# Performance work log

Hardware: AMD Instinct MI355X
Metric: run time of the kernel (lower is better)

The kernel has to match this reference:

```python
import jax, jax.numpy as jnp
import numpy as np

B, L, DIM = 2, 2048, 1024
H, DH, W = 16, 64, 256  # heads, head_dim, window_size
ROPE_BASE = 10000.0


def _rope(x):
    # x: [b, l, h, d] -> rotate consecutive pairs (torch view_as_complex semantics)
    l, d = x.shape[1], x.shape[3]
    freqs = 1.0 / (ROPE_BASE ** (jnp.arange(0, d, 2, dtype=jnp.float32) / d))  # [d/2]
    ang = jnp.arange(l, dtype=jnp.float32)[:, None] * freqs[None, :]           # [l, d/2]
    cos = jnp.cos(ang)[None, :, None, :].astype(x.dtype)
    sin = jnp.sin(ang)[None, :, None, :].astype(x.dtype)
    xe, xo = x[..., 0::2], x[..., 1::2]
    ye = xe * cos - xo * sin
    yo = xe * sin + xo * cos
    return jnp.stack([ye, yo], axis=-1).reshape(x.shape)


def setup_inputs() -> dict:
    key = jax.random.key(0)
    ks = jax.random.split(key, 7)
    sh = (B, L, DIM)
    return {
        "q": jax.random.normal(ks[0], sh, jnp.float32),
        "k": jax.random.normal(ks[1], sh, jnp.float32),
        "v": jax.random.normal(ks[2], sh, jnp.float32),
        "wq": jax.random.normal(ks[3], (H * DH, DIM), jnp.float32) * 0.02,
        "wk": jax.random.normal(ks[4], (H * DH, DIM), jnp.float32) * 0.02,
        "wv": jax.random.normal(ks[5], (H * DH, DIM), jnp.float32) * 0.02,
        "wo": jax.random.normal(ks[6], (DIM, H * DH), jnp.float32) * 0.02,
    }


def reference(q, k, v, wq, wk, wv, wo):
    b, l, _ = q.shape
    qh = (q @ wq.T).reshape(b, l, H, DH)
    kh = (k @ wk.T).reshape(b, l, H, DH)
    vh = (v @ wv.T).reshape(b, l, H, DH).transpose(0, 2, 1, 3)  # [b,h,l,d]
    qh = _rope(qh).transpose(0, 2, 1, 3)                        # [b,h,l,d]
    kh = _rope(kh).transpose(0, 2, 1, 3)
    scores = jnp.einsum('bhqd,bhkd->bhqk', qh, kh) * (DH ** -0.5)
    i = jnp.arange(l)[:, None]
    j = jnp.arange(l)[None, :]
    window_mask = (j <= i) & (j >= i - W)  # keys in [i-W, i], matches the loop
    scores = jnp.where(window_mask, scores, -1e30)
    probs = jax.nn.softmax(scores, axis=-1)
    out = jnp.einsum('bhqk,bhkd->bhqd', probs, vh)
    out = out.transpose(0, 2, 1, 3).reshape(b, l, H * DH)
    return out @ wo.T
```

## Files before the change

kernel.cpp:

```cpp
#include <hip/hip_runtime.h>
#include <stdint.h>

#define B_    2
#define L_    2048
#define DIM_  1024
#define H_    16
#define DH_   64
#define WWIN  256

typedef __attribute__((ext_vector_type(4))) float f32x4;
typedef __attribute__((ext_vector_type(8))) short bf16x8;

__device__ __forceinline__ unsigned short f2bf(float x) {
  union { float f; unsigned u; } c; c.f = x;
  unsigned r = c.u + 0x7fffu + ((c.u >> 16) & 1u);
  return (unsigned short)(r >> 16);
}

struct CastArgs {
  const float* src[7];
  unsigned short* dst[7];
};
__global__ __launch_bounds__(256) void cast_bf16_kernel(CastArgs a) {
  int bid = blockIdx.x;
  int arr, base;
  if (bid < 12288) {
    arr = bid >> 12;
    base = (bid & 4095) << 10;
  } else {
    int t = bid - 12288;
    arr = 3 + (t >> 10);
    base = (t & 1023) << 10;
  }
  int i = base + (int)threadIdx.x * 4;
  float4 v = *(const float4*)(a.src[arr] + i);
  ushort4 o;
  o.x = f2bf(v.x); o.y = f2bf(v.y); o.z = f2bf(v.z); o.w = f2bf(v.w);
  *(ushort4*)(a.dst[arr] + i) = o;
}

#define BM 128
#define BN 64
#define BK 64

__device__ __forceinline__ void gld_lds16(const void* g, void* l) {
  __builtin_amdgcn_global_load_lds(
      (const __attribute__((address_space(1))) void*)g,
      (__attribute__((address_space(3))) void*)l, 16, 0, 0);
}

__device__ __forceinline__ void gemm_core_1024(
    const unsigned short* __restrict__ A, const unsigned short* __restrict__ Bt,
    unsigned short* As, unsigned short* Bs, f32x4 (&acc)[2][4],
    int m0, int n0) {
  const int tid = threadIdx.x;
  const int wave = tid >> 6, lane = tid & 63;
  const int quad = lane >> 4, l16 = lane & 15;
  const int srow = tid >> 3, sc = tid & 7;

  auto stage = [&](int k0, int buf) {
    unsigned short* Ad = As + buf * 8192;
    unsigned short* Bd = Bs + buf * 4096;
    #pragma unroll
    for (int rd = 0; rd < 4; ++rd) {
      int row = rd * 32 + srow;
      int cs = sc ^ (row & 7);
      gld_lds16(A + (size_t)(m0 + row) * 1024 + k0 + cs * 8, Ad + row * BK + sc * 8);
    }
    #pragma unroll
    for (int rd = 0; rd < 2; ++rd) {
      int row = rd * 32 + srow;
      int cs = sc ^ (row & 7);
      gld_lds16(Bt + (size_t)(n0 + row) * 1024 + k0 + cs * 8, Bd + row * BK + sc * 8);
    }
  };

  stage(0, 0);
  for (int k = 0; k < 16; ++k) {
    const int cur = k & 1;
    __syncthreads();
    if (k < 15) stage((k + 1) * BK, cur ^ 1);
    const unsigned short* Ac = As + cur * 8192;
    const unsigned short* Bc = Bs + cur * 4096;
    #pragma unroll
    for (int ks = 0; ks < 2; ++ks) {
      bf16x8 af[2], bfr[4];
      #pragma unroll
      for (int i = 0; i < 2; ++i) {
        int row = wave * 32 + i * 16 + l16;
        int ch = (ks * 4 + quad) ^ (row & 7);
        af[i] = *(const bf16x8*)(Ac + row * BK + ch * 8);
      }
      #pragma unroll
      for (int j = 0; j < 4; ++j) {
        int row = j * 16 + l16;
        int ch = (ks * 4 + quad) ^ (row & 7);
        bfr[j] = *(const bf16x8*)(Bc + row * BK + ch * 8);
      }
      #pragma unroll
      for (int i = 0; i < 2; ++i)
        #pragma unroll
        for (int j = 0; j < 4; ++j)
          acc[i][j] = __builtin_amdgcn_mfma_f32_16x16x32_bf16(af[i], bfr[j], acc[i][j], 0, 0, 0);
    }
  }
}

struct ProjArgs {
  const unsigned short* A[3];
  const unsigned short* Bt[3];
  unsigned short* C[3];
};
__global__ __launch_bounds__(256) void gemm_proj_kernel(ProjArgs pa) {
  __shared__ unsigned short SH[24576];
  unsigned short* As = SH;
  unsigned short* Bs = SH + 16384;

  const int bflat = blockIdx.x;
  const int xcd = bflat & 7, s = bflat >> 3;
  const int nblk = s & 15;
  const int mz = xcd * 12 + (s >> 4);
  const int z = mz >> 5;
  const int mblk = mz & 31;
  const int m0 = mblk * BM, n0 = nblk * BN;

  f32x4 acc[2][4] = {};
  gemm_core_1024(pa.A[z], pa.Bt[z], As, Bs, acc, m0, n0);

  const int tid = threadIdx.x;
  const int lane = tid & 63, wave = tid >> 6;
  const int quad = lane >> 4, l16 = lane & 15;

  if (z < 2) {
    float frev[4];
    #pragma unroll
    for (int j = 0; j < 4; ++j) {
      int d = j * 16 + l16;
      frev[j] = exp2f(-(float)(d >> 1) * 0.41524101186092029f) * 0.15915494309189535f;
    }
    unsigned short* C = pa.C[z];
    const int h = nblk;
    const bool even = (l16 & 1) == 0;
    #pragma unroll
    for (int i = 0; i < 2; ++i)
      #pragma unroll
      for (int r = 0; r < 4; ++r) {
        int m = m0 + wave * 32 + i * 16 + quad * 4 + r;
        int b = m >> 11, l = m & (L_ - 1);
        float lf = (float)l;
        #pragma unroll
        for (int j = 0; j < 4; ++j) {
          int d = j * 16 + l16;
          float v = acc[i][j][r];
          float p = __shfl_xor(v, 1);
          float a = lf * frev[j];
          float t = a - floorf(a);
          float sn = __builtin_amdgcn_sinf(t);
          float cs = __builtin_amdgcn_cosf(t);
          float o = even ? (v * cs - p * sn) : (p * sn + v * cs);
          C[(((size_t)b * H_ + h) * L_ + l) * DH_ + d] = f2bf(o);
        }
      }
  } else {
    __syncthreads();
    unsigned short* T = SH + wave * 2304;
    #pragma unroll
    for (int i = 0; i < 2; ++i)
      #pragma unroll
      for (int j = 0; j < 4; ++j) {
        int nw = j * 16 + l16;
        int hm = i * 4 + quad;
        uint2 pk;
        pk.x = (unsigned)f2bf(acc[i][j][0]) | ((unsigned)f2bf(acc[i][j][1]) << 16);
        pk.y = (unsigned)f2bf(acc[i][j][2]) | ((unsigned)f2bf(acc[i][j][3]) << 16);
        *(uint2*)(T + nw * 36 + hm * 4) = pk;
      }
    asm volatile("s_waitcnt lgkmcnt(0)" ::: "memory");
    int h = nblk;
    int d = lane;
    int b = m0 >> 11;
    int lbase = (m0 & (L_ - 1)) + wave * 32;
    unsigned short* C = pa.C[2];
    size_t rowbase = (((size_t)b * H_ + h) * DH_ + d) * L_ + lbase;
    #pragma unroll
    for (int t = 0; t < 4; ++t) {
      uint2 lo = *(uint2*)(T + lane * 36 + t * 8);
      uint2 hi = *(uint2*)(T + lane * 36 + t * 8 + 4);
      uint4 o = {lo.x, lo.y, hi.x, hi.y};
      *(uint4*)(C + rowbase + t * 8) = o;
    }
  }
}

__global__ __launch_bounds__(256) void gemm_out_kernel(
    const unsigned short* __restrict__ A, const unsigned short* __restrict__ Bt,
    float* __restrict__ C) {
  __shared__ unsigned short SH[24576];
  unsigned short* As = SH;
  unsigned short* Bs = SH + 16384;

  const int bflat = blockIdx.x;
  const int xcd = bflat & 7, s = bflat >> 3;
  const int nblk = s & 15;
  const int mblk = xcd * 4 + (s >> 4);
  const int m0 = mblk * BM, n0 = nblk * BN;

  f32x4 acc[2][4] = {};
  gemm_core_1024(A, Bt, As, Bs, acc, m0, n0);

  const int lane = threadIdx.x & 63, wave = threadIdx.x >> 6;
  const int quad = lane >> 4, l16 = lane & 15;
  #pragma unroll
  for (int i = 0; i < 2; ++i)
    #pragma unroll
    for (int j = 0; j < 4; ++j)
      #pragma unroll
      for (int r = 0; r < 4; ++r) {
        int m = m0 + wave * 32 + i * 16 + quad * 4 + r;
        int n = n0 + j * 16 + l16;
        C[(size_t)m * DIM_ + n] = acc[i][j][r];
      }
}

#define VSTR 336
__global__ __launch_bounds__(256) void attn_kernel(
    const unsigned short* __restrict__ Qh,
    const unsigned short* __restrict__ Kh,
    const unsigned short* __restrict__ Vt,
    unsigned short* __restrict__ O) {
  __shared__ unsigned short Vs[64 * VSTR];
  const int tid = threadIdx.x;
  const int wave = tid >> 6, lane = tid & 63;
  const int quad = lane >> 4, l16 = lane & 15;

  const int bflat = blockIdx.x;
  const int xcd = bflat & 7, s = bflat >> 3;
  const int qt = s >> 2;
  const int bh = xcd * 4 + (s & 3);

  const int q0 = qt * 64;
  const int qb = q0 + wave * 16;
  const int kw0 = qb - WWIN;
  const bool edge = (kw0 < 0);

  const unsigned short* vbase = Vt + (size_t)bh * DH_ * L_;
  #pragma unroll
  for (int it = 0; it < 11; ++it) {
    if (it * 256 + wave * 64 < 2688) {
      int ci = it * 256 + tid;
      int row = ci / 42, ch = ci - row * 42;
      int key0 = q0 - WWIN + ch * 8;
      key0 = key0 < 0 ? 0 : key0;
      key0 = key0 > (L_ - 8) ? (L_ - 8) : key0;
      gld_lds16(vbase + (size_t)row * L_ + key0, Vs + ci * 8);
    }
  }

  bf16x8 qf0, qf1;
  {
    const unsigned short* qrow = Qh + ((size_t)bh * L_ + qb + l16) * DH_;
    qf0 = *(const bf16x8*)(qrow + quad * 8);
    qf1 = *(const bf16x8*)(qrow + 32 + quad * 8);
  }

  f32x4 S[17] = {};
  const unsigned short* kbase = Kh + (size_t)bh * L_ * DH_;
  #pragma unroll
  for (int c = 0; c < 17; ++c) {
    int key = kw0 + c * 16 + l16;
    key = key < 0 ? 0 : key;
    const unsigned short* kr = kbase + (size_t)key * DH_ + quad * 8;
    bf16x8 kf0 = *(const bf16x8*)(kr);
    bf16x8 kf1 = *(const bf16x8*)(kr + 32);
    S[c] = __builtin_amdgcn_mfma_f32_16x16x32_bf16(kf0, qf0, S[c], 0, 0, 0);
    S[c] = __builtin_amdgcn_mfma_f32_16x16x32_bf16(kf1, qf1, S[c], 0, 0, 0);
  }

  const int off16 = quad * 4;
  #pragma unroll
  for (int r = 0; r < 4; ++r) {
    if (off16 + r < l16)  S[0][r]  = -1e30f;
    if (off16 + r > l16)  S[16][r] = -1e30f;
  }
  if (edge) {
    #pragma unroll
    for (int c = 0; c < 17; ++c)
      #pragma unroll
      for (int r = 0; r < 4; ++r)
        if (kw0 + c * 16 + off16 + r < 0) S[c][r] = -1e30f;
  }

  float mx = -1e30f;
  #pragma unroll
  for (int c = 0; c < 17; ++c)
    #pragma unroll
    for (int r = 0; r < 4; ++r)
      mx = fmaxf(mx, S[c][r]);
  mx = fmaxf(mx, __shfl_xor(mx, 16));
  mx = fmaxf(mx, __shfl_xor(mx, 32));
  float sum = 0.f;
  #pragma unroll
  for (int c = 0; c < 17; ++c)
    #pragma unroll
    for (int r = 0; r < 4; ++r) {
      float e = __builtin_amdgcn_exp2f((S[c][r] - mx) * 0.18033688011112042f);
      S[c][r] = e;
      sum += e;
    }
  sum += __shfl_xor(sum, 16);
  sum += __shfl_xor(sum, 32);
  const float ivl = 1.0f / sum;

  __syncthreads();

  f32x4 Oacc[4] = {};
  const int srcA = (lane & 15) | ((lane & 16) << 1);
  const int srcB = srcA + 16;
  const bool loq = quad < 2;
  #pragma unroll
  for (int g = 0; g < 9; ++g) {
    unsigned uA0, uA1, uB0, uB1;
    {
      float a0 = S[2 * g][0] * ivl, a1 = S[2 * g][1] * ivl;
      float a2 = S[2 * g][2] * ivl, a3 = S[2 * g][3] * ivl;
      asm("v_cvt_pk_bf16_f32 %0, %1, %2" : "=v"(uA0) : "v"(a0), "v"(a1));
      asm("v_cvt_pk_bf16_f32 %0, %1, %2" : "=v"(uA1) : "v"(a2), "v"(a3));
    }
    if (g < 8) {
      float b0 = S[2 * g + 1][0] * ivl, b1 = S[2 * g + 1][1] * ivl;
      float b2 = S[2 * g + 1][2] * ivl, b3 = S[2 * g + 1][3] * ivl;
      asm("v_cvt_pk_bf16_f32 %0, %1, %2" : "=v"(uB0) : "v"(b0), "v"(b1));
      asm("v_cvt_pk_bf16_f32 %0, %1, %2" : "=v"(uB1) : "v"(b2), "v"(b3));
    } else {
      uB0 = 0; uB1 = 0;
    }
    unsigned tA0a = __shfl(uA0, srcA), tA1a = __shfl(uA1, srcA);
    unsigned tB0a = __shfl(uB0, srcA), tB1a = __shfl(uB1, srcA);
    unsigned tA0b = __shfl(uA0, srcB), tA1b = __shfl(uA1, srcB);
    unsigned tB0b = __shfl(uB0, srcB), tB1b = __shfl(uB1, srcB);
    union { unsigned u[4]; bf16x8 v; } pa;
    pa.u[0] = loq ? tA0a : tB0a;
    pa.u[1] = loq ? tA1a : tB1a;
    pa.u[2] = loq ? tA0b : tB0b;
    pa.u[3] = loq ? tA1b : tB1b;
    const int kloc = wave * 16 + g * 32 + quad * 8;
    #pragma unroll
    for (int t = 0; t < 4; ++t) {
      bf16x8 vf = *(const bf16x8*)(&Vs[(t * 16 + l16) * VSTR + kloc]);
      Oacc[t] = __builtin_amdgcn_mfma_f32_16x16x32_bf16(pa.v, vf, Oacc[t], 0, 0, 0);
    }
  }

  int b = bh >> 4, h = bh & 15;
  #pragma unroll
  for (int t = 0; t < 4; ++t)
    #pragma unroll
    for (int r = 0; r < 4; ++r) {
      int l = qb + quad * 4 + r;
      int col = h * DH_ + t * 16 + l16;
      O[((size_t)b * L_ + l) * (H_ * DH_) + col] = f2bf(Oacc[t][r]);
    }
}

extern "C" void kernel_launch(void* const* d_in, const int* in_sizes, int n_in,
                              void* d_out, int out_size, void* d_ws, size_t ws_size,
                              hipStream_t stream) {
  const float* q  = (const float*)d_in[0];
  const float* k  = (const float*)d_in[1];
  const float* v  = (const float*)d_in[2];
  const float* wq = (const float*)d_in[3];
  const float* wk = (const float*)d_in[4];
  const float* wv = (const float*)d_in[5];
  const float* wo = (const float*)d_in[6];

  const size_t SA = (size_t)B_ * L_ * DIM_;
  const size_t SW = (size_t)DIM_ * DIM_;
  unsigned short* w   = (unsigned short*)d_ws;
  unsigned short* qb  = w; w += SA;
  unsigned short* kb  = w; w += SA;
  unsigned short* vb  = w; w += SA;
  unsigned short* wqb = w; w += SW;
  unsigned short* wkb = w; w += SW;
  unsigned short* wvb = w; w += SW;
  unsigned short* wob = w; w += SW;
  unsigned short* qh  = w; w += SA;
  unsigned short* kh  = w; w += SA;
  unsigned short* vt  = w; w += SA;
  unsigned short* Ob  = w; w += SA;

  CastArgs ca;
  ca.src[0] = q;  ca.dst[0] = qb;
  ca.src[1] = k;  ca.dst[1] = kb;
  ca.src[2] = v;  ca.dst[2] = vb;
  ca.src[3] = wq; ca.dst[3] = wqb;
  ca.src[4] = wk; ca.dst[4] = wkb;
  ca.src[5] = wv; ca.dst[5] = wvb;
  ca.src[6] = wo; ca.dst[6] = wob;
  cast_bf16_kernel<<<dim3(16384), 256, 0, stream>>>(ca);

  ProjArgs pa;
  pa.A[0] = qb; pa.Bt[0] = wqb; pa.C[0] = qh;
  pa.A[1] = kb; pa.Bt[1] = wkb; pa.C[1] = kh;
  pa.A[2] = vb; pa.Bt[2] = wvb; pa.C[2] = vt;
  gemm_proj_kernel<<<dim3(16 * 32 * 3), 256, 0, stream>>>(pa);

  attn_kernel<<<dim3(32 * 32), 256, 0, stream>>>(qh, kh, vt, Ob);
  gemm_out_kernel<<<dim3(16 * 32), 256, 0, stream>>>(Ob, wob, (float*)d_out);
}
```

Before: 183.6 us.

## Use 128x128 BK32 tiles for QKV projection and swizzle attention V tile

The QKV projection GEMM moves from 128x64 tiles with BK=64 to 128x128 tiles with BK=32 on a 2x2 wave grid. This halves the block count and doubles the reuse of each A tile, and the V-transpose epilogue is rewritten around an XOR-swizzled LDS staging area. The attention kernel's V tile in LDS drops its padded stride (336 to 320) and uses an XOR swizzle on chunk index to avoid bank conflicts, and the final g==8 chunk index is clamped. The cost is more accumulator registers per thread (64 floats), which may lower occupancy, and only 768 blocks to fill the device.

Result: slower. 189.6 us (+3.2%).

```diff
diff --git a/kernel.cpp b/kernel.cpp
--- a/kernel.cpp
+++ b/kernel.cpp
@@ -49,6 +49,62 @@
       (__attribute__((address_space(3))) void*)l, 16, 0, 0);
 }
 
+__device__ __forceinline__ void gemm_core_128x128_bk32(
+    const unsigned short* __restrict__ A, const unsigned short* __restrict__ Bt,
+    unsigned short* As, unsigned short* Bs, f32x4 (&acc)[4][4],
+    int m0, int n0) {
+  const int tid = threadIdx.x;
+  const int wave = tid >> 6, lane = tid & 63;
+  const int quad = lane >> 4, l16 = lane & 15;
+  const int wm = wave >> 1, wn = wave & 1;
+
+  auto stage = [&](int k0, int buf) {
+    unsigned short* Ad = As + buf * 4096;
+    unsigned short* Bd = Bs + buf * 4096;
+    #pragma unroll
+    for (int rd = 0; rd < 2; ++rd) {
+      int ci = rd * 256 + tid;
+      int row = ci >> 2, ch = ci & 3;
+      int gch = ch ^ (row & 3);
+      gld_lds16(A + (size_t)(m0 + row) * 1024 + k0 + gch * 8, Ad + ci * 8);
+    }
+    #pragma unroll
+    for (int rd = 0; rd < 2; ++rd) {
+      int ci = rd * 256 + tid;
+      int row = ci >> 2, ch = ci & 3;
+      int gch = ch ^ (row & 3);
+      gld_lds16(Bt + (size_t)(n0 + row) * 1024 + k0 + gch * 8, Bd + ci * 8);
+    }
+  };
+
+  stage(0, 0);
+  for (int k = 0; k < 32; ++k) {
+    const int cur = k & 1;
+    __syncthreads();
+    if (k < 31) stage((k + 1) * 32, cur ^ 1);
+    const unsigned short* Ac = As + cur * 4096;
+    const unsigned short* Bc = Bs + cur * 4096;
+    bf16x8 af[4], bfr[4];
+    #pragma unroll
+    for (int i = 0; i < 4; ++i) {
+      int row = wm * 64 + i * 16 + l16;
+      int slot = quad ^ (row & 3);
+      af[i] = *(const bf16x8*)(Ac + row * 32 + slot * 8);
+    }
+    #pragma unroll
+    for (int j = 0; j < 4; ++j) {
+      int row = wn * 64 + j * 16 + l16;
+      int slot = quad ^ (row & 3);
+      bfr[j] = *(const bf16x8*)(Bc + row * 32 + slot * 8);
+    }
+    #pragma unroll
+    for (int i = 0; i < 4; ++i)
+      #pragma unroll
+      for (int j = 0; j < 4; ++j)
+        acc[i][j] = __builtin_amdgcn_mfma_f32_16x16x32_bf16(af[i], bfr[j], acc[i][j], 0, 0, 0);
+  }
+}
+
 __device__ __forceinline__ void gemm_core_1024(
     const unsigned short* __restrict__ A, const unsigned short* __restrict__ Bt,
     unsigned short* As, unsigned short* Bs, f32x4 (&acc)[2][4],
@@ -112,24 +168,26 @@
   unsigned short* C[3];
 };
 __global__ __launch_bounds__(256) void gemm_proj_kernel(ProjArgs pa) {
-  __shared__ unsigned short SH[24576];
+  __shared__ unsigned short SH[16384];
   unsigned short* As = SH;
-  unsigned short* Bs = SH + 16384;
+  unsigned short* Bs = SH + 8192;
 
   const int bflat = blockIdx.x;
   const int xcd = bflat & 7, s = bflat >> 3;
-  const int nblk = s & 15;
-  const int mz = xcd * 12 + (s >> 4);
+  const int nblk = s & 7;
+  const int mz = xcd * 12 + (s >> 3);
   const int z = mz >> 5;
   const int mblk = mz & 31;
-  const int m0 = mblk * BM, n0 = nblk * BN;
-
-  f32x4 acc[2][4] = {};
-  gemm_core_1024(pa.A[z], pa.Bt[z], As, Bs, acc, m0, n0);
+  const int m0 = mblk * BM, n0 = nblk * 128;
+
+  f32x4 acc[4][4] = {};
+  gemm_core_128x128_bk32(pa.A[z], pa.Bt[z], As, Bs, acc, m0, n0);
 
   const int tid = threadIdx.x;
   const int lane = tid & 63, wave = tid >> 6;
   const int quad = lane >> 4, l16 = lane & 15;
+  const int wm = wave >> 1, wn = wave & 1;
+  const int h = nblk * 2 + wn;
 
   if (z < 2) {
     float frev[4];
@@ -139,13 +197,12 @@
       frev[j] = exp2f(-(float)(d >> 1) * 0.41524101186092029f) * 0.15915494309189535f;
     }
     unsigned short* C = pa.C[z];
-    const int h = nblk;
     const bool even = (l16 & 1) == 0;
     #pragma unroll
-    for (int i = 0; i < 2; ++i)
+    for (int i = 0; i < 4; ++i)
       #pragma unroll
       for (int r = 0; r < 4; ++r) {
-        int m = m0 + wave * 32 + i * 16 + quad * 4 + r;
+        int m = m0 + wm * 64 + i * 16 + quad * 4 + r;
         int b = m >> 11, l = m & (L_ - 1);
         float lf = (float)l;
         #pragma unroll
@@ -163,31 +220,29 @@
       }
   } else {
     __syncthreads();
-    unsigned short* T = SH + wave * 2304;
-    #pragma unroll
-    for (int i = 0; i < 2; ++i)
+    char* T = (char*)SH + wave * 8192;
+    #pragma unroll
+    for (int i = 0; i < 4; ++i)
       #pragma unroll
       for (int j = 0; j < 4; ++j) {
-        int nw = j * 16 + l16;
-        int hm = i * 4 + quad;
+        int d = j * 16 + l16;
+        int mb = i * 32 + quad * 8;
+        int ch = mb >> 4, sub = mb & 15;
         uint2 pk;
         pk.x = (unsigned)f2bf(acc[i][j][0]) | ((unsigned)f2bf(acc[i][j][1]) << 16);
         pk.y = (unsigned)f2bf(acc[i][j][2]) | ((unsigned)f2bf(acc[i][j][3]) << 16);
-        *(uint2*)(T + nw * 36 + hm * 4) = pk;
+        *(uint2*)(T + d * 128 + ((ch ^ (d & 7)) << 4) + sub) = pk;
       }
     asm volatile("s_waitcnt lgkmcnt(0)" ::: "memory");
-    int h = nblk;
-    int d = lane;
     int b = m0 >> 11;
-    int lbase = (m0 & (L_ - 1)) + wave * 32;
+    int lbase = (m0 & (L_ - 1)) + wm * 64;
     unsigned short* C = pa.C[2];
-    size_t rowbase = (((size_t)b * H_ + h) * DH_ + d) * L_ + lbase;
-    #pragma unroll
-    for (int t = 0; t < 4; ++t) {
-      uint2 lo = *(uint2*)(T + lane * 36 + t * 8);
-      uint2 hi = *(uint2*)(T + lane * 36 + t * 8 + 4);
-      uint4 o = {lo.x, lo.y, hi.x, hi.y};
-      *(uint4*)(C + rowbase + t * 8) = o;
+    #pragma unroll
+    for (int t = 0; t < 8; ++t) {
+      int d = t * 8 + (lane >> 3);
+      int ch = lane & 7;
+      uint4 o = *(uint4*)(T + d * 128 + ((ch ^ (d & 7)) << 4));
+      *(uint4*)(C + (((size_t)b * H_ + h) * DH_ + d) * L_ + lbase + ch * 8) = o;
     }
   }
 }
@@ -222,7 +277,7 @@
       }
 }
 
-#define VSTR 336
+#define VSTR 320
 __global__ __launch_bounds__(256) void attn_kernel(
     const unsigned short* __restrict__ Qh,
     const unsigned short* __restrict__ Kh,
@@ -245,15 +300,13 @@
 
   const unsigned short* vbase = Vt + (size_t)bh * DH_ * L_;
   #pragma unroll
-  for (int it = 0; it < 11; ++it) {
-    if (it * 256 + wave * 64 < 2688) {
-      int ci = it * 256 + tid;
-      int row = ci / 42, ch = ci - row * 42;
-      int key0 = q0 - WWIN + ch * 8;
-      key0 = key0 < 0 ? 0 : key0;
-      key0 = key0 > (L_ - 8) ? (L_ - 8) : key0;
-      gld_lds16(vbase + (size_t)row * L_ + key0, Vs + ci * 8);
-    }
+  for (int it = 0; it < 10; ++it) {
+    int ci = it * 256 + tid;
+    int row = ci / 40, ch = ci - row * 40;
+    int gch = ch ^ (row & 7);
+    int key0 = q0 - WWIN + gch * 8;
+    key0 = key0 < 0 ? 0 : key0;
+    gld_lds16(vbase + (size_t)row * L_ + key0, Vs + ci * 8);
   }
 
   bf16x8 qf0, qf1;
@@ -338,16 +391,19 @@
     unsigned tB0a = __shfl(uB0, srcA), tB1a = __shfl(uB1, srcA);
     unsigned tA0b = __shfl(uA0, srcB), tA1b = __shfl(uA1, srcB);
     unsigned tB0b = __shfl(uB0, srcB), tB1b = __shfl(uB1, srcB);
-    union { unsigned u[4]; bf16x8 v; } pa;
-    pa.u[0] = loq ? tA0a : tB0a;
-    pa.u[1] = loq ? tA1a : tB1a;
-    pa.u[2] = loq ? tA0b : tB0b;
-    pa.u[3] = loq ? tA1b : tB1b;
-    const int kloc = wave * 16 + g * 32 + quad * 8;
+    union { unsigned u[4]; bf16x8 v; } pav;
+    pav.u[0] = loq ? tA0a : tB0a;
+    pav.u[1] = loq ? tA1a : tB1a;
+    pav.u[2] = loq ? tA0b : tB0b;
+    pav.u[3] = loq ? tA1b : tB1b;
+    int C = wave * 2 + g * 4 + quad;
+    if (g == 8) C = C > 39 ? 39 : C;
     #pragma unroll
     for (int t = 0; t < 4; ++t) {
-      bf16x8 vf = *(const bf16x8*)(&Vs[(t * 16 + l16) * VSTR + kloc]);
-      Oacc[t] = __builtin_amdgcn_mfma_f32_16x16x32_bf16(pa.v, vf, Oacc[t], 0, 0, 0);
+      int row = t * 16 + l16;
+      int slot = C ^ (row & 7);
+      bf16x8 vf = *(const bf16x8*)(&Vs[row * VSTR + slot * 8]);
+      Oacc[t] = __builtin_amdgcn_mfma_f32_16x16x32_bf16(pav.v, vf, Oacc[t], 0, 0, 0);
     }
   }
 
@@ -402,7 +458,7 @@
   pa.A[0] = qb; pa.Bt[0] = wqb; pa.C[0] = qh;
   pa.A[1] = kb; pa.Bt[1] = wkb; pa.C[1] = kh;
   pa.A[2] = vb; pa.Bt[2] = wvb; pa.C[2] = vt;
-  gemm_proj_kernel<<<dim3(16 * 32 * 3), 256, 0, stream>>>(pa);
+  gemm_proj_kernel<<<dim3(768), 256, 0, stream>>>(pa);
 
   attn_kernel<<<dim3(32 * 32), 256, 0, stream>>>(qh, kh, vt, Ob);
   gemm_out_kernel<<<dim3(16 * 32), 256, 0, stream>>>(Ob, wob, (float*)d_out);
```
